# Kernel optimization log

Hardware: AMD Instinct MI355X
Metric: run time of the kernel (lower is better)

## Reference

```python
import jax, jax.numpy as jnp
import numpy as np

# Network topology constants (topological order: inputs, L hidden layers, outputs)
N_IN = 512
H = 1024      # hidden nodes per layer
L = 8         # hidden layers
N_OUT = 256
DEG = 64      # enabled incoming connections per non-input node
B = 1024      # batch of input vectors

LAYER_SIZES = [H] * L + [N_OUT]
E_TOTAL = sum(n * DEG for n in LAYER_SIZES)  # 540672


def setup_inputs() -> dict:
    key = jax.random.key(0)
    k_in, k_w = jax.random.split(key)
    inputs = jax.random.normal(k_in, (B, N_IN), dtype=jnp.float32)
    # scale weights ~1/sqrt(DEG) so sigmoid pre-activations are well-conditioned
    weights = jax.random.normal(k_w, (E_TOTAL,), dtype=jnp.float32) / np.sqrt(DEG)
    # src indices: for each layer, incoming edges may come from ANY earlier node
    rng = np.random.default_rng(0)
    src_chunks = []
    n_before = N_IN
    for n in LAYER_SIZES:
        src_chunks.append(rng.integers(0, n_before, size=n * DEG))
        n_before += n
    src_idx = jnp.asarray(np.concatenate(src_chunks), dtype=jnp.int32)
    return {"inputs": inputs, "weights": weights, "src_idx": src_idx}


def reference(inputs, weights, src_idx):
    # outs: [B, n_nodes_evaluated_so_far], grown layer by layer (topological order)
    outs = inputs
    off = 0
    for n in LAYER_SIZES:
        e = n * DEG
        s = src_idx[off:off + e]            # [e] gather indices into earlier nodes
        w = weights[off:off + e]            # [e]
        gathered = outs[:, s] * w           # [B, e] irregular gather + scale
        z = gathered.reshape(-1, n, DEG).sum(-1)  # per-node sum over DEG in-edges
        outs = jnp.concatenate([outs, jax.nn.sigmoid(z)], axis=1)
        off += e
    return outs[:, -N_OUT:]  # [B, N_OUT] outputs of 'output' nodes
```

## Files before the change

kernel.cpp:

```cpp
#include <hip/hip_runtime.h>
#include <math.h>


#define N_IN    512
#define NLAYER  9
#define DEG     64
#define BATCH   1024
#define BPB     4
#define THREADS 1024
#define TOTAL_N 8960
#define N_OUT   256
#define NEDGE_N 8448

union H4 { uint2 u; _Float16 h[4]; };
union H2 { unsigned u; _Float16 h[2]; };
union HS { _Float16 h; unsigned short s; };

__global__ __launch_bounds__(256)
void neat_prep(const float* __restrict__ wts,
               const int*   __restrict__ sidx,
               uint4*       __restrict__ rec)
{
    __shared__ unsigned sortbuf[4][64];

    const int tid  = threadIdx.x;
    const int wave = tid >> 6;
    const int lane = tid & 63;
    const int t    = blockIdx.x * 4 + wave;
    const unsigned long long lt = (1ull << lane) - 1ull;

    const int e   = (t << 6) + lane;
    const int idx = sidx[e];
    HS w; w.h = (_Float16)wts[e];
    const int c = idx & 15;

    unsigned long long m[16];
    #pragma unroll
    for (int cc = 0; cc < 16; ++cc) m[cc] = __ballot(c == cc);

    int rank = 0, spillbefore = 0;
    #pragma unroll
    for (int cc = 0; cc < 16; ++cc) {
        const int n = (int)__popcll(m[cc]);
        if (cc == c) rank = (int)__popcll(m[cc] & lt);
        spillbefore += (cc < c && n > 4) ? (n - 4) : 0;
    }
    const bool spill = (rank >= 4);
    int slot_pre = spill ? -1 : ((c << 2) + rank);
    const int myspill = spillbefore + rank - 4;

    int hcum = 0;
    #pragma unroll
    for (int cc = 0; cc < 16; ++cc) {
        const int n = (int)__popcll(m[cc]);
        int holes = 4 - n; holes = holes > 0 ? holes : 0;
        const bool take = (slot_pre < 0) && (myspill < hcum + holes);
        slot_pre = take ? ((cc << 2) + n + (myspill - hcum)) : slot_pre;
        hcum += holes;
    }

    const int fl    = t & 63;
    const int sigma = ((fl & 15) << 2) | (fl >> 4);
    const int slot  = (slot_pre + sigma) & 63;
    sortbuf[wave][slot] = (unsigned)idx | ((unsigned)w.s << 16);
    __syncthreads();

    if (lane < 16) {
        const unsigned s0 = sortbuf[wave][(lane << 2) + 0];
        const unsigned s1 = sortbuf[wave][(lane << 2) + 1];
        const unsigned s2 = sortbuf[wave][(lane << 2) + 2];
        const unsigned s3 = sortbuf[wave][(lane << 2) + 3];
        uint4 o;
        o.x = (s0 & 0xffffu) | (s1 << 16);
        o.y = (s2 & 0xffffu) | (s3 << 16);
        o.z = (s0 >> 16) | (s1 & 0xffff0000u);
        o.w = (s2 >> 16) | (s3 & 0xffff0000u);
        rec[((t >> 6) << 10) + (lane << 6) + fl] = o;
    }
}

__global__ __launch_bounds__(THREADS, 4)
void neat_fwd(const float* __restrict__ in,
              const uint4* __restrict__ rec,
              float*       __restrict__ out)
{
    __shared__ _Float16 act[TOTAL_N * BPB];

    const int tid   = threadIdx.x;
    const int bbase = blockIdx.x * BPB;

    {
        const float* src = in + bbase * N_IN;
        for (int t = tid; t < BPB * N_IN; t += THREADS) {
            int j = t >> 9;
            int i = t & (N_IN - 1);
            act[i * BPB + j] = (_Float16)src[t];
        }
    }
    __syncthreads();

    int recBase = 0;
    int nb      = N_IN;
    #pragma unroll 1
    for (int layer = 0; layer < NLAYER; ++layer) {
        const int n = (layer < NLAYER - 1) ? 1024 : N_OUT;
        if (tid < n) {
            const int neuron = tid;
            const uint4* rp = rec + recBase + ((neuron >> 6) << 10) + (neuron & 63);

            uint4 r[16];
            #pragma unroll
            for (int q = 0; q < 16; ++q) r[q] = rp[q << 6];

            float4 acc = make_float4(0.f, 0.f, 0.f, 0.f);
            #pragma unroll
            for (int q = 0; q < 16; ++q) {
                const uint4 r4 = r[q];
                H4 g0, g1, g2, g3;
                g0.u = *reinterpret_cast<const uint2*>(act + ((r4.x & 0xffffu) << 2));
                g1.u = *reinterpret_cast<const uint2*>(act + ((r4.x >> 16) << 2));
                g2.u = *reinterpret_cast<const uint2*>(act + ((r4.y & 0xffffu) << 2));
                g3.u = *reinterpret_cast<const uint2*>(act + ((r4.y >> 16) << 2));
                H2 wz, ww; wz.u = r4.z; ww.u = r4.w;
                const float w0 = (float)wz.h[0];
                const float w1 = (float)wz.h[1];
                const float w2 = (float)ww.h[0];
                const float w3 = (float)ww.h[1];
                acc.x = fmaf((float)g0.h[0], w0, acc.x);
                acc.y = fmaf((float)g0.h[1], w0, acc.y);
                acc.z = fmaf((float)g0.h[2], w0, acc.z);
                acc.w = fmaf((float)g0.h[3], w0, acc.w);
                acc.x = fmaf((float)g1.h[0], w1, acc.x);
                acc.y = fmaf((float)g1.h[1], w1, acc.y);
                acc.z = fmaf((float)g1.h[2], w1, acc.z);
                acc.w = fmaf((float)g1.h[3], w1, acc.w);
                acc.x = fmaf((float)g2.h[0], w2, acc.x);
                acc.y = fmaf((float)g2.h[1], w2, acc.y);
                acc.z = fmaf((float)g2.h[2], w2, acc.z);
                acc.w = fmaf((float)g2.h[3], w2, acc.w);
                acc.x = fmaf((float)g3.h[0], w3, acc.x);
                acc.y = fmaf((float)g3.h[1], w3, acc.y);
                acc.z = fmaf((float)g3.h[2], w3, acc.z);
                acc.w = fmaf((float)g3.h[3], w3, acc.w);
            }

            float4 sg;
            sg.x = 1.f / (1.f + __expf(-acc.x));
            sg.y = 1.f / (1.f + __expf(-acc.y));
            sg.z = 1.f / (1.f + __expf(-acc.z));
            sg.w = 1.f / (1.f + __expf(-acc.w));

            if (layer < NLAYER - 1) {
                H4 p;
                p.h[0] = (_Float16)sg.x; p.h[1] = (_Float16)sg.y;
                p.h[2] = (_Float16)sg.z; p.h[3] = (_Float16)sg.w;
                *reinterpret_cast<uint2*>(act + ((nb + neuron) << 2)) = p.u;
            } else {
                float* op = out + neuron;
                op[(bbase + 0) * N_OUT] = sg.x;
                op[(bbase + 1) * N_OUT] = sg.y;
                op[(bbase + 2) * N_OUT] = sg.z;
                op[(bbase + 3) * N_OUT] = sg.w;
            }
        }
        __syncthreads();
        recBase += n << 4;
        nb      += n;
    }
}

extern "C" void kernel_launch(void* const* d_in, const int* in_sizes, int n_in,
                              void* d_out, int out_size, void* d_ws, size_t ws_size,
                              hipStream_t stream)
{
    const float* in  = (const float*)d_in[0];
    const float* wts = (const float*)d_in[1];
    const int*   sx  = (const int*)d_in[2];
    float*       out = (float*)d_out;
    uint4*       rec = (uint4*)d_ws;

    neat_prep<<<NEDGE_N / 4, 256, 0, stream>>>(wts, sx, rec);
    neat_fwd<<<BATCH / BPB, THREADS, 0, stream>>>(in, rec, out);
}
```

Before: 49.49 us.

## Duplicate activations in a swizzled LDS copy to reduce gather bank conflicts

Each activation is stored twice in shared memory: once in the original layout and once at a position swizzled within each group of 16. The prep kernel assigns every edge to whichever copy gives it a free bank-class slot, so each wave's gathers spread more evenly across LDS banks. Shared memory per block doubles to about 140KB, which may limit how many blocks fit per CU. Every activation write also becomes two stores, and the prep kernel does more ballot work.

```diff
diff --git a/kernel.cpp b/kernel.cpp
--- a/kernel.cpp
+++ b/kernel.cpp
@@ -16,6 +16,10 @@
 union H2 { unsigned u; _Float16 h[2]; };
 union HS { _Float16 h; unsigned short s; };
 
+__device__ __forceinline__ int jswz(int i) {
+    return (i & ~15) | ((i + (i >> 4)) & 15);
+}
+
 __global__ __launch_bounds__(256)
 void neat_prep(const float* __restrict__ wts,
                const int*   __restrict__ sidx,
@@ -32,37 +36,51 @@
     const int e   = (t << 6) + lane;
     const int idx = sidx[e];
     HS w; w.h = (_Float16)wts[e];
-    const int c = idx & 15;
-
-    unsigned long long m[16];
+    const int cA = idx & 15;
+    const int cB = (idx + (idx >> 4)) & 15;
+
+    unsigned long long mA[16];
     #pragma unroll
-    for (int cc = 0; cc < 16; ++cc) m[cc] = __ballot(c == cc);
-
-    int rank = 0, spillbefore = 0;
+    for (int cc = 0; cc < 16; ++cc) mA[cc] = __ballot(cA == cc);
+    const int rankA = (int)__popcll(mA[cA] & lt);
+    const bool accA = rankA < 4;
+
+    unsigned long long mB[16];
     #pragma unroll
-    for (int cc = 0; cc < 16; ++cc) {
-        const int n = (int)__popcll(m[cc]);
-        if (cc == c) rank = (int)__popcll(m[cc] & lt);
-        spillbefore += (cc < c && n > 4) ? (n - 4) : 0;
-    }
-    const bool spill = (rank >= 4);
-    int slot_pre = spill ? -1 : ((c << 2) + rank);
-    const int myspill = spillbefore + rank - 4;
-
-    int hcum = 0;
-    #pragma unroll
-    for (int cc = 0; cc < 16; ++cc) {
-        const int n = (int)__popcll(m[cc]);
-        int holes = 4 - n; holes = holes > 0 ? holes : 0;
-        const bool take = (slot_pre < 0) && (myspill < hcum + holes);
-        slot_pre = take ? ((cc << 2) + n + (myspill - hcum)) : slot_pre;
-        hcum += holes;
-    }
+    for (int cc = 0; cc < 16; ++cc) mB[cc] = __ballot(!accA && cB == cc);
+    int uAcB = (int)__popcll(mA[cB]); uAcB = uAcB < 4 ? uAcB : 4;
+    const int rankB = (int)__popcll(mB[cB] & lt);
+    const bool accB = !accA && (rankB < 4 - uAcB);
+
+    const bool placed = accA || accB;
+    int slot_pre;
+    if (placed) {
+        slot_pre = accA ? ((cA << 2) + rankA) : ((cB << 2) + uAcB + rankB);
+    } else {
+        const unsigned long long msp = __ballot(!placed);
+        const int myspill = (int)__popcll(msp & lt);
+        int hcum = 0; slot_pre = 0;
+        bool found = false;
+        #pragma unroll
+        for (int cc = 0; cc < 16; ++cc) {
+            int uA = (int)__popcll(mA[cc]); uA = uA < 4 ? uA : 4;
+            int uB = (int)__popcll(mB[cc]); const int capB = 4 - uA;
+            uB = uB < capB ? uB : capB;
+            const int used  = uA + uB;
+            const int holes = 4 - used;
+            const bool take = !found && (myspill < hcum + holes);
+            slot_pre = take ? ((cc << 2) + used + (myspill - hcum)) : slot_pre;
+            found = found || take;
+            hcum += holes;
+        }
+    }
+
+    const int v = accB ? (8960 + jswz(idx)) : idx;
 
     const int fl    = t & 63;
     const int sigma = ((fl & 15) << 2) | (fl >> 4);
     const int slot  = (slot_pre + sigma) & 63;
-    sortbuf[wave][slot] = (unsigned)idx | ((unsigned)w.s << 16);
+    sortbuf[wave][slot] = (unsigned)v | ((unsigned)w.s << 16);
     __syncthreads();
 
     if (lane < 16) {
@@ -84,7 +102,7 @@
               const uint4* __restrict__ rec,
               float*       __restrict__ out)
 {
-    __shared__ _Float16 act[TOTAL_N * BPB];
+    __shared__ _Float16 act[2 * TOTAL_N * BPB];
 
     const int tid   = threadIdx.x;
     const int bbase = blockIdx.x * BPB;
@@ -94,7 +112,9 @@
         for (int t = tid; t < BPB * N_IN; t += THREADS) {
             int j = t >> 9;
             int i = t & (N_IN - 1);
-            act[i * BPB + j] = (_Float16)src[t];
+            const _Float16 v = (_Float16)src[t];
+            act[(i << 2) + j] = v;
+            act[((8960 + jswz(i)) << 2) + j] = v;
         }
     }
     __syncthreads();
@@ -112,7 +132,7 @@
             #pragma unroll
             for (int q = 0; q < 16; ++q) r[q] = rp[q << 6];
 
-            float4 acc = make_float4(0.f, 0.f, 0.f, 0.f);
+            float accx = 0.f, accy = 0.f, accz = 0.f, accw = 0.f;
             #pragma unroll
             for (int q = 0; q < 16; ++q) {
                 const uint4 r4 = r[q];
@@ -126,35 +146,37 @@
                 const float w1 = (float)wz.h[1];
                 const float w2 = (float)ww.h[0];
                 const float w3 = (float)ww.h[1];
-                acc.x = fmaf((float)g0.h[0], w0, acc.x);
-                acc.y = fmaf((float)g0.h[1], w0, acc.y);
-                acc.z = fmaf((float)g0.h[2], w0, acc.z);
-                acc.w = fmaf((float)g0.h[3], w0, acc.w);
-                acc.x = fmaf((float)g1.h[0], w1, acc.x);
-                acc.y = fmaf((float)g1.h[1], w1, acc.y);
-                acc.z = fmaf((float)g1.h[2], w1, acc.z);
-                acc.w = fmaf((float)g1.h[3], w1, acc.w);
-                acc.x = fmaf((float)g2.h[0], w2, acc.x);
-                acc.y = fmaf((float)g2.h[1], w2, acc.y);
-                acc.z = fmaf((float)g2.h[2], w2, acc.z);
-                acc.w = fmaf((float)g2.h[3], w2, acc.w);
-                acc.x = fmaf((float)g3.h[0], w3, acc.x);
-                acc.y = fmaf((float)g3.h[1], w3, acc.y);
-                acc.z = fmaf((float)g3.h[2], w3, acc.z);
-                acc.w = fmaf((float)g3.h[3], w3, acc.w);
+                accx = fmaf((float)g0.h[0], w0, accx);
+                accy = fmaf((float)g0.h[1], w0, accy);
+                accz = fmaf((float)g0.h[2], w0, accz);
+                accw = fmaf((float)g0.h[3], w0, accw);
+                accx = fmaf((float)g1.h[0], w1, accx);
+                accy = fmaf((float)g1.h[1], w1, accy);
+                accz = fmaf((float)g1.h[2], w1, accz);
+                accw = fmaf((float)g1.h[3], w1, accw);
+                accx = fmaf((float)g2.h[0], w2, accx);
+                accy = fmaf((float)g2.h[1], w2, accy);
+                accz = fmaf((float)g2.h[2], w2, accz);
+                accw = fmaf((float)g2.h[3], w2, accw);
+                accx = fmaf((float)g3.h[0], w3, accx);
+                accy = fmaf((float)g3.h[1], w3, accy);
+                accz = fmaf((float)g3.h[2], w3, accz);
+                accw = fmaf((float)g3.h[3], w3, accw);
             }
 
             float4 sg;
-            sg.x = 1.f / (1.f + __expf(-acc.x));
-            sg.y = 1.f / (1.f + __expf(-acc.y));
-            sg.z = 1.f / (1.f + __expf(-acc.z));
-            sg.w = 1.f / (1.f + __expf(-acc.w));
+            sg.x = 1.f / (1.f + __expf(-accx));
+            sg.y = 1.f / (1.f + __expf(-accy));
+            sg.z = 1.f / (1.f + __expf(-accz));
+            sg.w = 1.f / (1.f + __expf(-accw));
 
             if (layer < NLAYER - 1) {
                 H4 p;
                 p.h[0] = (_Float16)sg.x; p.h[1] = (_Float16)sg.y;
                 p.h[2] = (_Float16)sg.z; p.h[3] = (_Float16)sg.w;
-                *reinterpret_cast<uint2*>(act + ((nb + neuron) << 2)) = p.u;
+                const int no = nb + neuron;
+                *reinterpret_cast<uint2*>(act + (no << 2)) = p.u;
+                *reinterpret_cast<uint2*>(act + ((8960 + jswz(no)) << 2)) = p.u;
             } else {
                 float* op = out + neuron;
                 op[(bbase + 0) * N_OUT] = sg.x;
```

Result: slower. 51.68 us (+4.4%).
